# Kernel tuning notes

Hardware: AMD Instinct MI355X
Metric: run time of the kernel (lower is better)

The kernel has to match this reference:

```python
import jax, jax.numpy as jnp
import numpy as np

L, D, N_HEADS = 4096, 1024, 16
HEAD_D = D // N_HEADS


def setup_inputs() -> dict:
    key = jax.random.key(0)
    kx, kq, kbq, ko, kbo = jax.random.split(key, 5)
    lim_in = 1.0 / np.sqrt(D)
    return {
        "x": jax.random.normal(kx, (L, D), dtype=jnp.float32),
        # equinox nn.Linear(dim, 3*dim): weight [3D, D], bias [3D], uniform(-1/sqrt(in), 1/sqrt(in))
        "W_qkv": jax.random.uniform(kq, (3 * D, D), jnp.float32, -lim_in, lim_in),
        "b_qkv": jax.random.uniform(kbq, (3 * D,), jnp.float32, -lim_in, lim_in),
        "W_out": jax.random.uniform(ko, (D, D), jnp.float32, -lim_in, lim_in),
        "b_out": jax.random.uniform(kbo, (D,), jnp.float32, -lim_in, lim_in),
    }


def reference(x, W_qkv, b_qkv, W_out, b_out):
    # qkv projection: equinox Linear computes W @ x + b per token -> x @ W.T + b
    qkv = x @ W_qkv.T + b_qkv                         # [L, 3D]
    qkv = qkv.reshape(L, 3, N_HEADS, HEAD_D)
    qkv = jnp.transpose(qkv, (1, 2, 0, 3))            # [3, n, L, d]
    q, k, v = qkv[0], qkv[1], qkv[2]                  # each [n, L, d]

    scale = 1.0 / jnp.sqrt(jnp.asarray(HEAD_D, dtype=x.dtype))
    attn = jnp.einsum('nqd,nkd->nqk', q, k) * scale   # [n, L, L]
    causal = jnp.tril(jnp.ones((L, L), dtype=bool))
    attn = jnp.where(causal, attn, -jnp.inf)
    attn = jax.nn.softmax(attn, axis=-1)              # dropout rate 0 -> identity
    out = jnp.einsum('nqk,nkd->nqd', attn, v)         # [n, L, d]
    out = jnp.transpose(out, (1, 0, 2)).reshape(L, D)
    return out @ W_out.T + b_out                      # [L, D]
```

## Files before the change

kernel.cpp:

```cpp
#include <hip/hip_runtime.h>
#include <hip/hip_bf16.h>
#include <math.h>

#define L_SEQ 4096
#define DIM   1024
#define NH    16
#define HD    64

#define QSCL 0.18033688011112042f

typedef __attribute__((ext_vector_type(4)))  float f32x4;
typedef __attribute__((ext_vector_type(16))) float f32x16;
typedef __attribute__((ext_vector_type(8)))  short s16x8;
typedef __attribute__((ext_vector_type(4)))  short s16x4;
typedef __attribute__((ext_vector_type(4)))  unsigned u32x4;
typedef __attribute__((ext_vector_type(2)))  unsigned u32x2;

#if defined(__has_builtin)
#  if __has_builtin(__builtin_amdgcn_permlane32_swap)
#    define HAVE_PLSWAP 1
#  else
#    define HAVE_PLSWAP 0
#  endif
#else
#  define HAVE_PLSWAP 0
#endif

__device__ __forceinline__ short f2bf(float f) {
  unsigned u = __builtin_bit_cast(unsigned, f);
  u = u + 0x7fffu + ((u >> 16) & 1u);
  return (short)(u >> 16);
}

__device__ __forceinline__ unsigned cvt_pk_bf16(float lo, float hi_) {
  unsigned r;
  asm("v_cvt_pk_bf16_f32 %0, %1, %2" : "=v"(r) : "v"(lo), "v"(hi_));
  return r;
}

__device__ __forceinline__ float exp2_fast(float x) {
  float r;
  asm("v_exp_f32 %0, %1" : "=v"(r) : "v"(x));
  return r;
}

__device__ __forceinline__ void gload_lds16(const void* g, void* l) {
  __builtin_amdgcn_global_load_lds(
      (__attribute__((address_space(1))) void*)(g),
      (__attribute__((address_space(3))) void*)(l), 16, 0, 0);
}

#define CVT_N1 (L_SEQ * DIM / 4)
#define CVT_N2 (3 * DIM * DIM / 4)
#define CVT_N3 (DIM * DIM / 4)

__global__ __launch_bounds__(256) void cvt_all(const float* __restrict__ x,
                                               const float* __restrict__ Wqkv,
                                               const float* __restrict__ Wout,
                                               short* __restrict__ xb,
                                               short* __restrict__ wqkvb,
                                               short* __restrict__ woutb) {
  int i = blockIdx.x * 256 + threadIdx.x;
  const float* src;
  short* dst;
  int j;
  if (i < CVT_N1)               { src = x;    dst = xb;    j = i; }
  else if (i < CVT_N1 + CVT_N2) { src = Wqkv; dst = wqkvb; j = i - CVT_N1; }
  else                          { src = Wout; dst = woutb; j = i - CVT_N1 - CVT_N2; }
  f32x4 f = *(const f32x4*)(src + j * 4);
  s16x4 o;
  o[0] = f2bf(f[0]); o[1] = f2bf(f[1]); o[2] = f2bf(f[2]); o[3] = f2bf(f[3]);
  *(s16x4*)(dst + j * 4) = o;
}


#define GEMM_MAINLOOP(A_, B_, Kdim)                                            \
  f32x4 acc[4][4];                                                             \
  _Pragma("unroll") for (int m = 0; m < 4; ++m)                                \
  _Pragma("unroll") for (int n = 0; n < 4; ++n) acc[m][n] = (f32x4)0.f;        \
  const short* aptr = A_ + (bm * 128 + w * 16 + (l >> 2)) * (Kdim) + (l & 3) * 8; \
  const short* bptr = B_ + (bn * 128 + w * 16 + (l >> 2)) * (Kdim) + (l & 3) * 8; \
  short* asl = &As[(w * 16) * 32];                                             \
  short* bsl = &Bs[(w * 16) * 32];                                             \
  for (int kk = 0; kk < (Kdim); kk += 32) {                                    \
    gload_lds16(aptr + kk, asl);                                               \
    gload_lds16(aptr + kk + 64 * (Kdim), asl + 64 * 32);                       \
    gload_lds16(bptr + kk, bsl);                                               \
    gload_lds16(bptr + kk + 64 * (Kdim), bsl + 64 * 32);                       \
    __syncthreads();                                                           \
    s16x8 af[4], bfr[4];                                                       \
    _Pragma("unroll") for (int m = 0; m < 4; ++m)                              \
      af[m] = *(const s16x8*)&As[(wr * 64 + m * 16 + lr) * 32 + lg * 8];       \
    _Pragma("unroll") for (int n = 0; n < 4; ++n)                              \
      bfr[n] = *(const s16x8*)&Bs[(wc * 64 + n * 16 + lr) * 32 + lg * 8];      \
    _Pragma("unroll") for (int m = 0; m < 4; ++m)                              \
    _Pragma("unroll") for (int n = 0; n < 4; ++n)                              \
      acc[m][n] = __builtin_amdgcn_mfma_f32_16x16x32_bf16(af[m], bfr[n], acc[m][n], 0, 0, 0); \
    __syncthreads();                                                           \
  }

__global__ __launch_bounds__(256) void gemm_qkv(const short* __restrict__ A,
                                                const short* __restrict__ B,
                                                const float* __restrict__ bias,
                                                short* __restrict__ Qb,
                                                short* __restrict__ Kf,
                                                short* __restrict__ Vf) {
  __shared__ __align__(16) short As[128 * 32];
  __shared__ __align__(16) short Bs[128 * 32];
  const int t = threadIdx.x;
  const int w = t >> 6, l = t & 63;
  const int wr = w >> 1, wc = w & 1;
  const int lr = l & 15, lg = l >> 4;
  const int bid = blockIdx.x;
  const int xcd = bid & 7;
  const int ii = bid >> 3;
  const int bm = xcd * 4 + (ii & 3);
  const int bn = ii >> 2;

  GEMM_MAINLOOP(A, B, DIM)

  const int row0 = bm * 128 + wr * 64;
  const int col0 = bn * 128 + wc * 64;
#pragma unroll
  for (int n = 0; n < 4; ++n) {
    const int col = col0 + n * 16 + lr;
    const float bv = bias[col];
    const int which = col >> 10;
    const int head = (col & 1023) >> 6;
    const int d = col & 63;
    if (which == 0) {
      short* dst = Qb + (head * L_SEQ) * HD + d;
#pragma unroll
      for (int m = 0; m < 4; ++m)
#pragma unroll
        for (int j = 0; j < 4; ++j) {
          const int row = row0 + m * 16 + lg * 4 + j;
          dst[row * HD] = f2bf((acc[m][n][j] + bv) * QSCL);
        }
    } else if (which == 1) {
      const int c = d >> 4, khi = (d >> 3) & 1, e = d & 7;
      short* dst = Kf + head * (L_SEQ * HD);
#pragma unroll
      for (int m = 0; m < 4; ++m)
#pragma unroll
        for (int j = 0; j < 4; ++j) {
          const int row = row0 + m * 16 + lg * 4 + j;
          const int p = row >> 5;
          const int lane = khi * 32 + (row & 31);
          dst[((p * 4 + c) * 64 + lane) * 8 + e] = f2bf(acc[m][n][j] + bv);
        }
    } else {
      const int dh = d >> 5;
      const int dq = d & 31;
      short* dst = Vf + head * (L_SEQ * HD);
#pragma unroll
      for (int m = 0; m < 4; ++m) {
        const int rowb = row0 + m * 16 + lg * 4;
        const int tt = rowb >> 6;
        const int kc = (rowb >> 4) & 3;
        const int khi = (rowb >> 3) & 1;
        const int e0 = rowb & 7;
        s16x4 wv;
#pragma unroll
        for (int j = 0; j < 4; ++j) wv[j] = f2bf(acc[m][n][j] + bv);
        *(s16x4*)&dst[(((tt * 4 + kc) * 2 + dh) * 64 + khi * 32 + dq) * 8 + e0] = wv;
      }
    }
  }
}

__global__ __launch_bounds__(256) void gemm_out64(const short* __restrict__ A,
                                                  const short* __restrict__ B,
                                                  const float* __restrict__ bias,
                                                  float* __restrict__ C) {
  __shared__ __align__(16) short As[64 * 32];
  __shared__ __align__(16) short Bs[64 * 32];
  const int t = threadIdx.x;
  const int w = t >> 6, l = t & 63;
  const int wr = w >> 1, wc = w & 1;
  const int lr = l & 15, lg = l >> 4;
  const int bid = blockIdx.x;
  const int xcd = bid & 7;
  const int ii = bid >> 3;
  const int bm = xcd * 8 + (ii & 7);
  const int bn = ii >> 3;

  f32x4 acc[2][2];
#pragma unroll
  for (int m = 0; m < 2; ++m)
#pragma unroll
    for (int n = 0; n < 2; ++n) acc[m][n] = (f32x4)0.f;

  const short* aptr = A + (bm * 64 + (t >> 2)) * DIM + (t & 3) * 8;
  const short* bptr = B + (bn * 64 + (t >> 2)) * DIM + (t & 3) * 8;
  short* asl = &As[t * 8];
  short* bsl = &Bs[t * 8];

  for (int kk = 0; kk < DIM; kk += 32) {
    gload_lds16(aptr + kk, asl);
    gload_lds16(bptr + kk, bsl);
    __syncthreads();
    s16x8 af[2], bfr[2];
#pragma unroll
    for (int m = 0; m < 2; ++m)
      af[m] = *(const s16x8*)&As[(wr * 32 + m * 16 + lr) * 32 + lg * 8];
#pragma unroll
    for (int n = 0; n < 2; ++n)
      bfr[n] = *(const s16x8*)&Bs[(wc * 32 + n * 16 + lr) * 32 + lg * 8];
#pragma unroll
    for (int m = 0; m < 2; ++m)
#pragma unroll
      for (int n = 0; n < 2; ++n)
        acc[m][n] = __builtin_amdgcn_mfma_f32_16x16x32_bf16(af[m], bfr[n], acc[m][n], 0, 0, 0);
    __syncthreads();
  }

  const int row0 = bm * 64 + wr * 32;
  const int col0 = bn * 64 + wc * 32;
#pragma unroll
  for (int n = 0; n < 2; ++n) {
    const int col = col0 + n * 16 + lr;
    const float bv = bias[col];
#pragma unroll
    for (int m = 0; m < 2; ++m)
#pragma unroll
      for (int j = 0; j < 4; ++j) {
        const int row = row0 + m * 16 + lg * 4 + j;
        C[row * DIM + col] = acc[m][n][j] + bv;
      }
  }
}

__global__ __launch_bounds__(256, 4) void attn32(const short* __restrict__ Qb,
                                                 const short* __restrict__ Kf,
                                                 const short* __restrict__ Vf,
                                                 short* __restrict__ Ob) {
  __shared__ unsigned Ms[3][64][17];
  const int bid = blockIdx.x;
  const int xcd = bid & 7;
  const int idx = bid >> 3;
  const int head = (xcd << 1) | (idx & 1);
  const int pr = idx >> 1;
  const int h = threadIdx.x >> 6;
  const int l = threadIdx.x & 63;
  const int q = l & 31;
  const int hi = l >> 5;

  const short* Qh = Qb + head * (L_SEQ * HD);
  const short* Kh = Kf + head * (L_SEQ * HD);
  const short* Vh = Vf + head * (L_SEQ * HD);

#pragma unroll 1
  for (int ph = 0; ph < 2; ++ph) {
    const int qtile = ph ? pr : (127 - pr);
    const int q0 = qtile * 32;
    const int nkt = qtile + 1;

    s16x8 qf[4];
#pragma unroll
    for (int c = 0; c < 4; ++c)
      qf[c] = *(const s16x8*)&Qh[(q0 + q) * HD + c * 16 + hi * 8];

    f32x16 o0 = (f32x16)0.f, o1 = (f32x16)0.f;
    f32x4 lvec = (f32x4)0.f;

    s16x8 kf[4];
#pragma unroll
    for (int c = 0; c < 4; ++c)
      kf[c] = *(const s16x8*)&Kh[((h * 4 + c) * 64 + l) * 8];

    for (int kt = h; kt < nkt; kt += 4) {
      s16x8 vf[2][2];
#pragma unroll
      for (int cc = 0; cc < 2; ++cc)
#pragma unroll
        for (int dh = 0; dh < 2; ++dh)
          vf[cc][dh] = *(const s16x8*)&Vh[(((kt * 2 + cc) * 2 + dh) * 64 + l) * 8];

      f32x16 s = (f32x16)0.f;
      __builtin_amdgcn_s_setprio(1);
#pragma unroll
      for (int c = 0; c < 4; ++c)
        s = __builtin_amdgcn_mfma_f32_32x32x16_bf16(kf[c], qf[c], s, 0, 0, 0);
      __builtin_amdgcn_s_setprio(0);

      const int ktn = (kt + 4 < nkt) ? kt + 4 : kt;
#pragma unroll
      for (int c = 0; c < 4; ++c)
        kf[c] = *(const s16x8*)&Kh[((ktn * 4 + c) * 64 + l) * 8];

      if (kt == qtile) {
        const int qrel = q - hi * 4;
#pragma unroll
        for (int r = 0; r < 16; ++r) {
          const int koff = (r & 3) + 8 * (r >> 2);
          if (koff > qrel) s[r] = -1e30f;
        }
      }

#pragma unroll
      for (int r = 0; r < 16; ++r) s[r] = exp2_fast(s[r]);
#pragma unroll
      for (int r = 0; r < 16; ++r) lvec[r & 3] += s[r];

#pragma unroll
      for (int cc = 0; cc < 2; ++cc) {
        const int roff = cc * 8;
        const unsigned A = cvt_pk_bf16(s[roff + 0], s[roff + 1]);
        const unsigned B = cvt_pk_bf16(s[roff + 2], s[roff + 3]);
        const unsigned C = cvt_pk_bf16(s[roff + 4], s[roff + 5]);
        const unsigned D = cvt_pk_bf16(s[roff + 6], s[roff + 7]);
        u32x4 pw;
#if HAVE_PLSWAP
        const u32x2 r02 = __builtin_amdgcn_permlane32_swap(A, C, false, false);
        const u32x2 r13 = __builtin_amdgcn_permlane32_swap(B, D, false, false);
        pw[0] = r02[0]; pw[1] = r13[0]; pw[2] = r02[1]; pw[3] = r13[1];
#else
        const unsigned sA = (unsigned)__shfl_xor((int)A, 32, 64);
        const unsigned sB = (unsigned)__shfl_xor((int)B, 32, 64);
        const unsigned sC = (unsigned)__shfl_xor((int)C, 32, 64);
        const unsigned sD = (unsigned)__shfl_xor((int)D, 32, 64);
        pw[0] = hi ? sC : A;
        pw[1] = hi ? sD : B;
        pw[2] = hi ? C : sA;
        pw[3] = hi ? D : sB;
#endif
        const s16x8 pf = __builtin_bit_cast(s16x8, pw);
        __builtin_amdgcn_s_setprio(1);
        o0 = __builtin_amdgcn_mfma_f32_32x32x16_bf16(vf[cc][0], pf, o0, 0, 0, 0);
        o1 = __builtin_amdgcn_mfma_f32_32x32x16_bf16(vf[cc][1], pf, o1, 0, 0, 0);
        __builtin_amdgcn_s_setprio(0);
      }
    }

    float lsum = (lvec[0] + lvec[1]) + (lvec[2] + lvec[3]);
    lsum += __shfl_xor(lsum, 32, 64);

    if (h > 0) {
      unsigned* st = &Ms[h - 1][l][0];
#pragma unroll
      for (int w2 = 0; w2 < 8; ++w2) st[w2]     = cvt_pk_bf16(o0[2 * w2], o0[2 * w2 + 1]);
#pragma unroll
      for (int w2 = 0; w2 < 8; ++w2) st[8 + w2] = cvt_pk_bf16(o1[2 * w2], o1[2 * w2 + 1]);
      st[16] = __builtin_bit_cast(unsigned, lsum);
    }
    __syncthreads();
    if (h == 0) {
#pragma unroll
      for (int wv = 0; wv < 3; ++wv) {
        const unsigned* st = &Ms[wv][l][0];
        lsum += __builtin_bit_cast(float, st[16]);
#pragma unroll
        for (int w2 = 0; w2 < 8; ++w2) {
          const unsigned ua = st[w2];
          o0[2 * w2]     += __builtin_bit_cast(float, ua << 16);
          o0[2 * w2 + 1] += __builtin_bit_cast(float, ua & 0xffff0000u);
          const unsigned ub = st[8 + w2];
          o1[2 * w2]     += __builtin_bit_cast(float, ub << 16);
          o1[2 * w2 + 1] += __builtin_bit_cast(float, ub & 0xffff0000u);
        }
      }
      const float inv = 1.f / lsum;
      const int orow = q0 + q;
#pragma unroll
      for (int dh = 0; dh < 2; ++dh) {
#pragma unroll
        for (int tq = 0; tq < 4; ++tq) {
          s16x4 wv;
#pragma unroll
          for (int j = 0; j < 4; ++j) {
            const int r = tq * 4 + j;
            const float ov = (dh == 0) ? o0[r] : o1[r];
            wv[j] = f2bf(ov * inv);
          }
          *(s16x4*)&Ob[orow * DIM + head * HD + dh * 32 + tq * 8 + hi * 4] = wv;
        }
      }
    }
    __syncthreads();
  }
}

extern "C" void kernel_launch(void* const* d_in, const int* in_sizes, int n_in,
                              void* d_out, int out_size, void* d_ws, size_t ws_size,
                              hipStream_t stream) {
  const float* x    = (const float*)d_in[0];
  const float* Wqkv = (const float*)d_in[1];
  const float* bqkv = (const float*)d_in[2];
  const float* Wout = (const float*)d_in[3];
  const float* bout = (const float*)d_in[4];
  float* out = (float*)d_out;

  char* ws = (char*)d_ws;
  short* xb    = (short*)(ws);
  short* wqkvb = (short*)(ws + (8u  << 20));
  short* woutb = (short*)(ws + (14u << 20));
  short* Qb    = (short*)(ws + (16u << 20));
  short* Kf    = (short*)(ws + (24u << 20));
  short* Vf    = (short*)(ws + (32u << 20));
  short* Ob    = (short*)(ws + (40u << 20));

  cvt_all<<<(CVT_N1 + CVT_N2 + CVT_N3) / 256, 256, 0, stream>>>(x, Wqkv, Wout, xb, wqkvb, woutb);

  gemm_qkv<<<768, 256, 0, stream>>>(xb, wqkvb, bqkv, Qb, Kf, Vf);
  attn32<<<1024, 256, 0, stream>>>(Qb, Kf, Vf, Ob);
  gemm_out64<<<1024, 256, 0, stream>>>(Ob, woutb, bout, out);
}
```

Before: 129.6 us.

## Use 64-row query tiles with double-buffered LDS staging of shared K/V

Restructures the attention kernel so each block owns a 64-row query tile, split into two 32-row sub-blocks that are each processed by a pair of waves. K and V tiles are loaded asynchronously into a double-buffered LDS area and shared by all four waves, replacing per-wave direct global loads of K and V. This reduces global/L2 traffic by reusing each K/V tile across both query sub-blocks. In exchange it adds a block-wide barrier on every iteration and an extra causal-mask wave, and it drops the earlier pairing of a long and a short tile inside each block, so load balancing now depends on how blocks are ordered.

```diff
diff --git a/kernel.cpp b/kernel.cpp
--- a/kernel.cpp
+++ b/kernel.cpp
@@ -231,77 +231,87 @@
   }
 }
 
-__global__ __launch_bounds__(256, 4) void attn32(const short* __restrict__ Qb,
+__global__ __launch_bounds__(256, 4) void attn64(const short* __restrict__ Qb,
                                                  const short* __restrict__ Kf,
                                                  const short* __restrict__ Vf,
                                                  short* __restrict__ Ob) {
-  __shared__ unsigned Ms[3][64][17];
+  __shared__ __align__(16) short KV[2][8192];
   const int bid = blockIdx.x;
   const int xcd = bid & 7;
-  const int idx = bid >> 3;
-  const int head = (xcd << 1) | (idx & 1);
-  const int pr = idx >> 1;
+  const int i = bid >> 3;
+  const int head = (xcd << 1) | (i >> 6);
+  const int j = i & 63;
+  const int qt = (j < 32) ? (63 - j) : (j - 32);
+  const int q0 = qt * 64;
   const int h = threadIdx.x >> 6;
   const int l = threadIdx.x & 63;
   const int q = l & 31;
   const int hi = l >> 5;
+  const int sb = h >> 1;
+  const int p = h & 1;
 
   const short* Qh = Qb + head * (L_SEQ * HD);
   const short* Kh = Kf + head * (L_SEQ * HD);
   const short* Vh = Vf + head * (L_SEQ * HD);
-
-#pragma unroll 1
-  for (int ph = 0; ph < 2; ++ph) {
-    const int qtile = ph ? pr : (127 - pr);
-    const int q0 = qtile * 32;
-    const int nkt = qtile + 1;
-
-    s16x8 qf[4];
-#pragma unroll
-    for (int c = 0; c < 4; ++c)
-      qf[c] = *(const s16x8*)&Qh[(q0 + q) * HD + c * 16 + hi * 8];
-
-    f32x16 o0 = (f32x16)0.f, o1 = (f32x16)0.f;
-    f32x4 lvec = (f32x4)0.f;
-
-    s16x8 kf[4];
-#pragma unroll
-    for (int c = 0; c < 4; ++c)
-      kf[c] = *(const s16x8*)&Kh[((h * 4 + c) * 64 + l) * 8];
-
-    for (int kt = h; kt < nkt; kt += 4) {
-      s16x8 vf[2][2];
-#pragma unroll
-      for (int cc = 0; cc < 2; ++cc)
-#pragma unroll
-        for (int dh = 0; dh < 2; ++dh)
-          vf[cc][dh] = *(const s16x8*)&Vh[(((kt * 2 + cc) * 2 + dh) * 64 + l) * 8];
+  const short* gKV = (h < 2) ? Kh : Vh;
+
+  s16x8 qf[4];
+#pragma unroll
+  for (int c = 0; c < 4; ++c)
+    qf[c] = *(const s16x8*)&Qh[(q0 + sb * 32 + q) * HD + c * 16 + hi * 8];
+
+  f32x16 o0 = (f32x16)0.f, o1 = (f32x16)0.f;
+  f32x4 lvec = (f32x4)0.f;
+
+  const int nr = qt + 1;
+
+  {
+    const short* gsrc = gKV + p * 2048;
+    short* lb = &KV[0][h * 2048];
+#pragma unroll
+    for (int c = 0; c < 4; ++c) gload_lds16(gsrc + c * 512 + l * 8, lb + c * 512);
+  }
+  __syncthreads();
+
+  for (int r = 0; r < nr; ++r) {
+    const int buf = r & 1;
+    if (r + 1 < nr) {
+      const short* gsrc = gKV + (2 * (r + 1) + p) * 2048;
+      short* lb = &KV[buf ^ 1][h * 2048];
+#pragma unroll
+      for (int c = 0; c < 4; ++c) gload_lds16(gsrc + c * 512 + l * 8, lb + c * 512);
+    }
+
+    const bool last = (r == nr - 1);
+    if (!(h == 1 && last)) {
+      const short* kb = &KV[buf][p * 2048];
+      const short* vb = &KV[buf][(2 + p) * 2048];
+
+      s16x8 kfr[4];
+#pragma unroll
+      for (int c = 0; c < 4; ++c)
+        kfr[c] = *(const s16x8*)&kb[c * 512 + l * 8];
 
       f32x16 s = (f32x16)0.f;
       __builtin_amdgcn_s_setprio(1);
 #pragma unroll
       for (int c = 0; c < 4; ++c)
-        s = __builtin_amdgcn_mfma_f32_32x32x16_bf16(kf[c], qf[c], s, 0, 0, 0);
+        s = __builtin_amdgcn_mfma_f32_32x32x16_bf16(kfr[c], qf[c], s, 0, 0, 0);
       __builtin_amdgcn_s_setprio(0);
 
-      const int ktn = (kt + 4 < nkt) ? kt + 4 : kt;
-#pragma unroll
-      for (int c = 0; c < 4; ++c)
-        kf[c] = *(const s16x8*)&Kh[((ktn * 4 + c) * 64 + l) * 8];
-
-      if (kt == qtile) {
+      if (last && (h == 0 || h == 3)) {
         const int qrel = q - hi * 4;
 #pragma unroll
-        for (int r = 0; r < 16; ++r) {
-          const int koff = (r & 3) + 8 * (r >> 2);
-          if (koff > qrel) s[r] = -1e30f;
+        for (int rr = 0; rr < 16; ++rr) {
+          const int koff = (rr & 3) + 8 * (rr >> 2);
+          if (koff > qrel) s[rr] = -1e30f;
         }
       }
 
 #pragma unroll
-      for (int r = 0; r < 16; ++r) s[r] = exp2_fast(s[r]);
-#pragma unroll
-      for (int r = 0; r < 16; ++r) lvec[r & 3] += s[r];
+      for (int rr = 0; rr < 16; ++rr) s[rr] = exp2_fast(s[rr]);
+#pragma unroll
+      for (int rr = 0; rr < 16; ++rr) lvec[rr & 3] += s[rr];
 
 #pragma unroll
       for (int cc = 0; cc < 2; ++cc) {
@@ -320,64 +330,62 @@
         const unsigned sB = (unsigned)__shfl_xor((int)B, 32, 64);
         const unsigned sC = (unsigned)__shfl_xor((int)C, 32, 64);
         const unsigned sD = (unsigned)__shfl_xor((int)D, 32, 64);
-        pw[0] = hi ? sC : A;
-        pw[1] = hi ? sD : B;
-        pw[2] = hi ? C : sA;
-        pw[3] = hi ? D : sB;
+        pw[0] = hi ? sC : A; pw[1] = hi ? sD : B;
+        pw[2] = hi ? C : sA; pw[3] = hi ? D : sB;
 #endif
         const s16x8 pf = __builtin_bit_cast(s16x8, pw);
+        const s16x8 vf0 = *(const s16x8*)&vb[(cc * 2 + 0) * 512 + l * 8];
+        const s16x8 vf1 = *(const s16x8*)&vb[(cc * 2 + 1) * 512 + l * 8];
         __builtin_amdgcn_s_setprio(1);
-        o0 = __builtin_amdgcn_mfma_f32_32x32x16_bf16(vf[cc][0], pf, o0, 0, 0, 0);
-        o1 = __builtin_amdgcn_mfma_f32_32x32x16_bf16(vf[cc][1], pf, o1, 0, 0, 0);
+        o0 = __builtin_amdgcn_mfma_f32_32x32x16_bf16(vf0, pf, o0, 0, 0, 0);
+        o1 = __builtin_amdgcn_mfma_f32_32x32x16_bf16(vf1, pf, o1, 0, 0, 0);
         __builtin_amdgcn_s_setprio(0);
       }
     }
-
-    float lsum = (lvec[0] + lvec[1]) + (lvec[2] + lvec[3]);
-    lsum += __shfl_xor(lsum, 32, 64);
-
-    if (h > 0) {
-      unsigned* st = &Ms[h - 1][l][0];
-#pragma unroll
-      for (int w2 = 0; w2 < 8; ++w2) st[w2]     = cvt_pk_bf16(o0[2 * w2], o0[2 * w2 + 1]);
-#pragma unroll
-      for (int w2 = 0; w2 < 8; ++w2) st[8 + w2] = cvt_pk_bf16(o1[2 * w2], o1[2 * w2 + 1]);
-      st[16] = __builtin_bit_cast(unsigned, lsum);
+    __syncthreads();
+  }
+
+  float lsum = (lvec[0] + lvec[1]) + (lvec[2] + lvec[3]);
+  lsum += __shfl_xor(lsum, 32, 64);
+
+  unsigned* Ms = (unsigned*)&KV[0][0];
+  if (p == 1) {
+    unsigned* st = Ms + (sb * 64 + l) * 17;
+#pragma unroll
+    for (int w2 = 0; w2 < 8; ++w2) st[w2]     = cvt_pk_bf16(o0[2 * w2], o0[2 * w2 + 1]);
+#pragma unroll
+    for (int w2 = 0; w2 < 8; ++w2) st[8 + w2] = cvt_pk_bf16(o1[2 * w2], o1[2 * w2 + 1]);
+    st[16] = __builtin_bit_cast(unsigned, lsum);
+  }
+  __syncthreads();
+  if (p == 0) {
+    const unsigned* st = Ms + (sb * 64 + l) * 17;
+    lsum += __builtin_bit_cast(float, st[16]);
+#pragma unroll
+    for (int w2 = 0; w2 < 8; ++w2) {
+      const unsigned ua = st[w2];
+      o0[2 * w2]     += __builtin_bit_cast(float, ua << 16);
+      o0[2 * w2 + 1] += __builtin_bit_cast(float, ua & 0xffff0000u);
+      const unsigned ub = st[8 + w2];
+      o1[2 * w2]     += __builtin_bit_cast(float, ub << 16);
+      o1[2 * w2 + 1] += __builtin_bit_cast(float, ub & 0xffff0000u);
     }
-    __syncthreads();
-    if (h == 0) {
-#pragma unroll
-      for (int wv = 0; wv < 3; ++wv) {
-        const unsigned* st = &Ms[wv][l][0];
-        lsum += __builtin_bit_cast(float, st[16]);
-#pragma unroll
-        for (int w2 = 0; w2 < 8; ++w2) {
-          const unsigned ua = st[w2];
-          o0[2 * w2]     += __builtin_bit_cast(float, ua << 16);
-          o0[2 * w2 + 1] += __builtin_bit_cast(float, ua & 0xffff0000u);
-          const unsigned ub = st[8 + w2];
-          o1[2 * w2]     += __builtin_bit_cast(float, ub << 16);
-          o1[2 * w2 + 1] += __builtin_bit_cast(float, ub & 0xffff0000u);
+    const float inv = 1.f / lsum;
+    const int orow = q0 + sb * 32 + q;
+#pragma unroll
+    for (int dh = 0; dh < 2; ++dh) {
+#pragma unroll
+      for (int tq = 0; tq < 4; ++tq) {
+        s16x4 wv;
+#pragma unroll
+        for (int jj = 0; jj < 4; ++jj) {
+          const int rr = tq * 4 + jj;
+          const float ov = (dh == 0) ? o0[rr] : o1[rr];
+          wv[jj] = f2bf(ov * inv);
         }
-      }
-      const float inv = 1.f / lsum;
-      const int orow = q0 + q;
-#pragma unroll
-      for (int dh = 0; dh < 2; ++dh) {
-#pragma unroll
-        for (int tq = 0; tq < 4; ++tq) {
-          s16x4 wv;
-#pragma unroll
-          for (int j = 0; j < 4; ++j) {
-            const int r = tq * 4 + j;
-            const float ov = (dh == 0) ? o0[r] : o1[r];
-            wv[j] = f2bf(ov * inv);
-          }
-          *(s16x4*)&Ob[orow * DIM + head * HD + dh * 32 + tq * 8 + hi * 4] = wv;
-        }
+        *(s16x4*)&Ob[orow * DIM + head * HD + dh * 32 + tq * 8 + hi * 4] = wv;
       }
     }
-    __syncthreads();
   }
 }
 
@@ -403,6 +411,6 @@
   cvt_all<<<(CVT_N1 + CVT_N2 + CVT_N3) / 256, 256, 0, stream>>>(x, Wqkv, Wout, xb, wqkvb, woutb);
 
   gemm_qkv<<<768, 256, 0, stream>>>(xb, wqkvb, bqkv, Qb, Kf, Vf);
-  attn32<<<1024, 256, 0, stream>>>(Qb, Kf, Vf, Ob);
+  attn64<<<1024, 256, 0, stream>>>(Qb, Kf, Vf, Ob);
   gemm_out64<<<1024, 256, 0, stream>>>(Ob, woutb, bout, out);
 }
```

Result: faster. 125.2 us (-3.4%).
